# Performance work log

Hardware: AMD Instinct MI355X
Metric: run time of the kernel (lower is better)

## Reference

```python
import jax, jax.numpy as jnp
import numpy as np

B, N, M = 2, 4096, 1024
QD, CD, H, DH = 512, 768, 8, 64
SCALE = DH ** -0.5


def setup_inputs() -> dict:
    key = jax.random.key(0)
    ks = jax.random.split(key, 8)
    return {
        "x": jax.random.normal(ks[0], (B, N, QD), jnp.float32),
        "context": jax.random.normal(ks[1], (B, M, CD), jnp.float32),
        "adapt": jax.random.normal(ks[2], (B, N, H * DH), jnp.float32),
        "Wq": jax.random.normal(ks[3], (QD, H * DH), jnp.float32) * (QD ** -0.5),
        "Wk": jax.random.normal(ks[4], (CD, H * DH), jnp.float32) * (CD ** -0.5),
        "Wv": jax.random.normal(ks[5], (CD, H * DH), jnp.float32) * (CD ** -0.5),
        "Wo": jax.random.normal(ks[6], (H * DH, QD), jnp.float32) * ((H * DH) ** -0.5),
        "bo": jnp.zeros((QD,), jnp.float32),
    }


def _split_heads(t):
    # [b, n, h*d] -> [b, h, n, d]
    b, n, _ = t.shape
    return t.reshape(b, n, H, DH).transpose(0, 2, 1, 3)


def reference(x, context, adapt, Wq, Wk, Wv, Wo, bo):
    q = _split_heads(x @ Wq)          # [b,h,n,d]
    k = _split_heads(context @ Wk)    # [b,h,m,d]
    v = _split_heads(context @ Wv)    # [b,h,m,d]

    sim = jnp.einsum('bhid,bhjd->bhij', q, k) * SCALE  # [b,h,n,m]
    attn = jax.nn.softmax(sim, axis=-1)
    # NOTE: module averages raw logits (sim) over heads, not softmax probs
    attention_probs_avg = sim.mean(axis=1)             # [b,n,m]
    out = jnp.einsum('bhij,bhjd->bhid', attn, v)       # [b,h,n,d]

    # adapt-query pass reusing k, v
    qa = _split_heads(adapt)
    sim_a = jnp.einsum('bhid,bhjd->bhij', qa, k) * SCALE
    attn_a = jax.nn.softmax(sim_a, axis=-1)
    out = out + jnp.einsum('bhij,bhjd->bhid', attn_a, v)

    out = out.transpose(0, 2, 1, 3).reshape(B, N, H * DH)  # merge heads
    return (out @ Wo + bo, attention_probs_avg)
```

## Files before the change

### kernel.cpp

```cpp
#include <hip/hip_runtime.h>

typedef __attribute__((ext_vector_type(8))) short bh8;
typedef __attribute__((ext_vector_type(4))) float f4;
typedef __attribute__((ext_vector_type(4))) unsigned short us4;
typedef __attribute__((ext_vector_type(4))) unsigned int u32x4;

__device__ __forceinline__ unsigned short rne_bf16(float x) {
  unsigned int u = __builtin_bit_cast(unsigned int, x);
  u += 0x7fffu + ((u >> 16) & 1u);
  return (unsigned short)(u >> 16);
}

__device__ __forceinline__ unsigned int cvt_pk_bf16(float lo, float hi) {
  unsigned int r;
  asm("v_cvt_pk_bf16_f32 %0, %1, %2" : "=v"(r) : "v"(lo), "v"(hi));
  return r;
}

__device__ __forceinline__ void gl_lds16(const void* g, void* l) {
  __builtin_amdgcn_global_load_lds(
      (const __attribute__((address_space(1))) void*)g,
      (__attribute__((address_space(3))) void*)l, 16, 0, 0);
}

__global__ __launch_bounds__(256) void prep_kernel(
    const float* __restrict__ x, unsigned short* __restrict__ xb,
    const float* __restrict__ context, unsigned short* __restrict__ cb,
    const float* __restrict__ Wq, const float* __restrict__ Wk,
    const float* __restrict__ Wv, const float* __restrict__ Wo,
    unsigned short* __restrict__ WqT, unsigned short* __restrict__ WkvT,
    unsigned short* __restrict__ WoT) {
  const int bid = blockIdx.x, tid = threadIdx.x;
  if (bid < 1024) {
    const int n40 = (8192 * 512) / 4, n41 = (2048 * 768) / 4;
    const int total = n40 + n41, stride = 1024 * 256;
    for (int i = bid * 256 + tid; i < total; i += stride) {
      const float* in = (i < n40) ? x : context;
      unsigned short* out = (i < n40) ? xb : cb;
      const int j = (i < n40) ? i : (i - n40);
      f4 v = *(const f4*)(in + (long)j * 4);
      us4 o;
#pragma unroll
      for (int e = 0; e < 4; ++e) o[e] = rne_bf16(v[e]);
      *(us4*)(out + (long)j * 4) = o;
    }
    return;
  }
  int u = bid - 1024;
  const float* in;
  unsigned short* out;
  int K;
  if (u < 256)       { in = Wq; out = WqT;               K = 512; }
  else if (u < 640)  { u -= 256; in = Wk; out = WkvT;    K = 768; }
  else if (u < 1024) { u -= 640; in = Wv; out = WkvT + 512L * 768; K = 768; }
  else               { u -= 1024; in = Wo; out = WoT;    K = 512; }
  const int N = 512;
  const int n0 = (u & 15) * 32, k0 = (u >> 4) * 32;
  __shared__ float t[32][33];
  const int tx = tid & 31, ty = tid >> 5;
#pragma unroll
  for (int r = 0; r < 32; r += 8)
    t[ty + r][tx] = in[(long)(k0 + ty + r) * N + n0 + tx];
  __syncthreads();
#pragma unroll
  for (int r = 0; r < 32; r += 8)
    out[(long)(n0 + ty + r) * K + k0 + tx] = rne_bf16(t[tx][ty + r]);
}

template <int MODE>
__device__ __forceinline__ void gemm_body(
    const unsigned short* __restrict__ A, const unsigned short* __restrict__ Bt,
    void* __restrict__ Cv, int K, int lda, int ldb, int ldc,
    long astr, long bstr, long cstr, float scale, const float* __restrict__ bias,
    int bx, int by, int bz) {
  __shared__ unsigned short As[2][16 * 512];
  __shared__ unsigned short Bs[2][16 * 512];
  const int tid = threadIdx.x, w = tid >> 6, l = tid & 63;
  const int c = l & 15, g = l >> 4;
  const int m0 = by * 128, n0 = bx * 128;
  const unsigned short* Ab = A + (long)bz * astr;
  const unsigned short* Bb = Bt + (long)bz * bstr;

  auto stage = [&](int buf, int kt) {
#pragma unroll
    for (int s = 0; s < 4; ++s) {
      const int idx = w * 4 + s;
      const int row = ((idx >> 1) & 7) * 16 + c;
      const int col = kt * 64 + (idx & 1) * 32 + g * 8;
      gl_lds16(Ab + (long)(m0 + row) * lda + col, (char*)&As[buf][0] + idx * 1024);
      gl_lds16(Bb + (long)(n0 + row) * ldb + col, (char*)&Bs[buf][0] + idx * 1024);
    }
  };

  f4 acc[4][4];
#pragma unroll
  for (int i = 0; i < 4; ++i)
#pragma unroll
    for (int j = 0; j < 4; ++j) acc[i][j] = (f4){0.f, 0.f, 0.f, 0.f};

  const int nkt = K >> 6;
  stage(0, 0);
  asm volatile("s_waitcnt vmcnt(0)" ::: "memory");
  __syncthreads();

  for (int kt = 0; kt < nkt; ++kt) {
    const int cur = kt & 1;
    if (kt + 1 < nkt) stage(cur ^ 1, kt + 1);
#pragma unroll
    for (int kk = 0; kk < 2; ++kk) {
      bh8 af[4], bfr[4];
#pragma unroll
      for (int i = 0; i < 4; ++i) {
        af[i] = *(const bh8*)((const char*)&As[cur][0] + (((w >> 1) * 8 + i * 2 + kk) * 1024) + l * 16);
        bfr[i] = *(const bh8*)((const char*)&Bs[cur][0] + (((w & 1) * 8 + i * 2 + kk) * 1024) + l * 16);
      }
#pragma unroll
      for (int i = 0; i < 4; ++i)
#pragma unroll
        for (int j = 0; j < 4; ++j)
          acc[i][j] = __builtin_amdgcn_mfma_f32_16x16x32_bf16(af[i], bfr[j], acc[i][j], 0, 0, 0);
    }
    if (kt + 1 < nkt) {
      asm volatile("s_waitcnt vmcnt(0)" ::: "memory");
      __syncthreads();
    }
  }

  const int rbase = m0 + (w >> 1) * 64, cbase = n0 + (w & 1) * 64;
#pragma unroll
  for (int i = 0; i < 4; ++i)
#pragma unroll
    for (int j = 0; j < 4; ++j)
#pragma unroll
      for (int r = 0; r < 4; ++r) {
        const long row = rbase + i * 16 + g * 4 + r;
        const long col = cbase + j * 16 + c;
        const float v = acc[i][j][r];
        if (MODE == 0) {
          ((unsigned short*)Cv + (long)bz * cstr)[row * ldc + col] = rne_bf16(v * scale);
        } else if (MODE == 1) {
          ((float*)Cv + (long)bz * cstr)[row * ldc + col] = v * scale;
        } else {
          ((float*)Cv)[row * ldc + col] = v + bias[col];
        }
      }
}

__global__ __launch_bounds__(256, 2) void gemm_qkv(
    const unsigned short* __restrict__ xb, const unsigned short* __restrict__ WqT,
    unsigned short* __restrict__ Qb,
    const unsigned short* __restrict__ cb, const unsigned short* __restrict__ WkvT,
    unsigned short* __restrict__ KVb, float cexp) {
  const int bid = blockIdx.x;
  const unsigned short *A, *Bt;
  unsigned short* C;
  int K, ldb_, ldc_, bx, by;
  float sc;
  if (bid < 256) {
    A = xb; Bt = WqT; C = Qb; K = 512; ldb_ = 512; ldc_ = 512;
    bx = bid & 3; by = bid >> 2; sc = cexp;
  } else {
    const int u = bid - 256;
    A = cb; Bt = WkvT; C = KVb; K = 768; ldb_ = 768; ldc_ = 1024;
    bx = u & 7; by = u >> 3; sc = 1.f;
  }
  gemm_body<0>(A, Bt, C, K, K, ldb_, ldc_, 0, 0, 0, sc, nullptr, bx, by, 0);
}

__global__ __launch_bounds__(256, 2) void probs_vt(
    const unsigned short* __restrict__ Qb, const unsigned short* __restrict__ KVb,
    float* __restrict__ out1, unsigned short* __restrict__ VTb, float avg_scale) {
  const int bid = blockIdx.x;
  if (bid >= 512) {
    const int u = bid - 512;
    const int j0 = (u & 63) * 32, d0 = (u >> 6) * 32;
    __shared__ unsigned short t[32][34];
    const int tx = threadIdx.x & 31, ty = threadIdx.x >> 5;
#pragma unroll
    for (int r = 0; r < 32; r += 8)
      t[ty + r][tx] = KVb[(long)(j0 + ty + r) * 1024 + 512 + d0 + tx];
    __syncthreads();
#pragma unroll
    for (int r = 0; r < 32; r += 8)
      VTb[(long)(d0 + ty + r) * 2048 + j0 + tx] = t[tx][ty + r];
    return;
  }
  gemm_body<1>(Qb, KVb, out1, 512, 512, 1024, 1024,
               4096L * 512, 1024L * 1024, 4096L * 1024, avg_scale, nullptr,
               bid & 7, (bid >> 3) & 31, bid >> 8);
}

__global__ __launch_bounds__(256, 2) void gemm_out(
    const unsigned short* __restrict__ Ob, const unsigned short* __restrict__ WoT,
    float* __restrict__ out0, const float* __restrict__ bias) {
  gemm_body<2>(Ob, WoT, out0, 512, 512, 512, 512, 0, 0, 0, 1.f, bias,
               blockIdx.x, blockIdx.y, 0);
}

__global__ __launch_bounds__(256, 4) void attn_kernel(
    const unsigned short* __restrict__ Qb, const float* __restrict__ adapt,
    const unsigned short* __restrict__ KV, const unsigned short* __restrict__ VT,
    unsigned short* __restrict__ Ob) {
  __shared__ unsigned short Ks[2][8 * 512];
  __shared__ unsigned short Vs[2][8 * 512];
  const int qt = blockIdx.y, h = blockIdx.x, b = blockIdx.z;
  const int tid = threadIdx.x, w = tid >> 6, l = tid & 63;
  const int c = l & 15, g = l >> 4;
  const float CEXP = 0.18033688011112042f;

  const unsigned short* Kg = KV + ((long)b * 1024) * 1024 + h * 64;
  const unsigned short* Vg = VT + (long)h * 64 * 2048 + b * 1024;

  auto stage = [&](int buf, int jt0) {
#pragma unroll
    for (int s = 0; s < 2; ++s) {
      const int idx = w * 2 + s;
      const int row = (idx >> 1) * 16 + c;
      const int col = (idx & 1) * 32 + g * 8;
      gl_lds16(Kg + ((long)jt0 * 64 + row) * 1024 + col, (char*)&Ks[buf][0] + idx * 1024);
      gl_lds16(Vg + (long)row * 2048 + jt0 * 64 + col, (char*)&Vs[buf][0] + idx * 1024);
    }
  };

  stage(0, 0);

  const long qrow = (long)b * 4096 + qt * 64 + w * 16 + c;
  bh8 qf[2][2];
#pragma unroll
  for (int kk = 0; kk < 2; ++kk) {
    const int col = h * 64 + kk * 32 + g * 8;
    qf[0][kk] = *(const bh8*)(Qb + qrow * 512 + col);
    const float* ap = adapt + qrow * 512 + col;
    f4 x0 = *(const f4*)ap, x1 = *(const f4*)(ap + 4);
    bh8 t;
#pragma unroll
    for (int e = 0; e < 4; ++e) {
      t[e] = (short)rne_bf16(x0[e] * CEXP);
      t[e + 4] = (short)rne_bf16(x1[e] * CEXP);
    }
    qf[1][kk] = t;
  }

  f4 psum[2];
  f4 accv[2][4];
#pragma unroll
  for (int qs = 0; qs < 2; ++qs) {
    psum[qs] = (f4){0.f, 0.f, 0.f, 0.f};
#pragma unroll
    for (int dt = 0; dt < 4; ++dt) accv[qs][dt] = (f4){0.f, 0.f, 0.f, 0.f};
  }

  asm volatile("s_waitcnt vmcnt(0)" ::: "memory");
  __syncthreads();

  auto make_pf = [&](const f4& s2k, const f4& s2k1) -> bh8 {
    unsigned int p0 = cvt_pk_bf16(s2k[0], s2k[1]);
    unsigned int p1 = cvt_pk_bf16(s2k[2], s2k[3]);
    unsigned int q0 = cvt_pk_bf16(s2k1[0], s2k1[1]);
    unsigned int q1 = cvt_pk_bf16(s2k1[2], s2k1[3]);
    asm("v_permlane32_swap_b32 %0, %1" : "+v"(p0), "+v"(q0));
    asm("v_permlane16_swap_b32 %0, %1" : "+v"(p0), "+v"(q0));
    asm("v_permlane32_swap_b32 %0, %1" : "+v"(p1), "+v"(q1));
    asm("v_permlane16_swap_b32 %0, %1" : "+v"(p1), "+v"(q1));
    u32x4 u = {p0, p1, q0, q1};
    return __builtin_bit_cast(bh8, u);
  };

  for (int jt0 = 0; jt0 < 16; ++jt0) {
    const int cur = jt0 & 1;
    if (jt0 < 15) stage(cur ^ 1, jt0 + 1);

    f4 s0[4], s1[4];
    __builtin_amdgcn_s_setprio(1);
#pragma unroll
    for (int jt = 0; jt < 4; ++jt) {
      bh8 k0 = *(const bh8*)((const char*)&Ks[cur][0] + (jt * 2 + 0) * 1024 + l * 16);
      bh8 k1 = *(const bh8*)((const char*)&Ks[cur][0] + (jt * 2 + 1) * 1024 + l * 16);
      s0[jt] = (f4){0.f, 0.f, 0.f, 0.f};
      s0[jt] = __builtin_amdgcn_mfma_f32_16x16x32_bf16(k0, qf[0][0], s0[jt], 0, 0, 0);
      s0[jt] = __builtin_amdgcn_mfma_f32_16x16x32_bf16(k1, qf[0][1], s0[jt], 0, 0, 0);
      s1[jt] = (f4){0.f, 0.f, 0.f, 0.f};
      s1[jt] = __builtin_amdgcn_mfma_f32_16x16x32_bf16(k0, qf[1][0], s1[jt], 0, 0, 0);
      s1[jt] = __builtin_amdgcn_mfma_f32_16x16x32_bf16(k1, qf[1][1], s1[jt], 0, 0, 0);
    }
    __builtin_amdgcn_s_setprio(0);

#pragma unroll
    for (int jt = 0; jt < 4; ++jt)
#pragma unroll
      for (int r = 0; r < 4; ++r) {
        s0[jt][r] = __builtin_amdgcn_exp2f(s0[jt][r]);
        s1[jt][r] = __builtin_amdgcn_exp2f(s1[jt][r]);
      }
#pragma unroll
    for (int jt = 0; jt < 4; ++jt) { psum[0] += s0[jt]; psum[1] += s1[jt]; }

    bh8 pf0[2], pf1[2];
#pragma unroll
    for (int kk = 0; kk < 2; ++kk) {
      pf0[kk] = make_pf(s0[2 * kk], s0[2 * kk + 1]);
      pf1[kk] = make_pf(s1[2 * kk], s1[2 * kk + 1]);
    }

    __builtin_amdgcn_s_setprio(1);
#pragma unroll
    for (int dt = 0; dt < 4; ++dt) {
      bh8 v0 = *(const bh8*)((const char*)&Vs[cur][0] + (dt * 2 + 0) * 1024 + l * 16);
      bh8 v1 = *(const bh8*)((const char*)&Vs[cur][0] + (dt * 2 + 1) * 1024 + l * 16);
      accv[0][dt] = __builtin_amdgcn_mfma_f32_16x16x32_bf16(v0, pf0[0], accv[0][dt], 0, 0, 0);
      accv[0][dt] = __builtin_amdgcn_mfma_f32_16x16x32_bf16(v1, pf0[1], accv[0][dt], 0, 0, 0);
      accv[1][dt] = __builtin_amdgcn_mfma_f32_16x16x32_bf16(v0, pf1[0], accv[1][dt], 0, 0, 0);
      accv[1][dt] = __builtin_amdgcn_mfma_f32_16x16x32_bf16(v1, pf1[1], accv[1][dt], 0, 0, 0);
    }
    __builtin_amdgcn_s_setprio(0);

    if (jt0 < 15) {
      asm volatile("s_waitcnt vmcnt(0)" ::: "memory");
      __syncthreads();
    }
  }

  float l0 = (psum[0][0] + psum[0][1]) + (psum[0][2] + psum[0][3]);
  l0 += __shfl_xor(l0, 16); l0 += __shfl_xor(l0, 32);
  float l1 = (psum[1][0] + psum[1][1]) + (psum[1][2] + psum[1][3]);
  l1 += __shfl_xor(l1, 16); l1 += __shfl_xor(l1, 32);
  const float i0 = 1.0f / l0, i1 = 1.0f / l1;
  const long orow = (long)b * 4096 + qt * 64 + w * 16 + c;
#pragma unroll
  for (int dt = 0; dt < 4; ++dt) {
    float v0 = accv[0][dt][0] * i0 + accv[1][dt][0] * i1;
    float v1 = accv[0][dt][1] * i0 + accv[1][dt][1] * i1;
    float v2 = accv[0][dt][2] * i0 + accv[1][dt][2] * i1;
    float v3 = accv[0][dt][3] * i0 + accv[1][dt][3] * i1;
    uint2 o;
    o.x = cvt_pk_bf16(v0, v1);
    o.y = cvt_pk_bf16(v2, v3);
    *(uint2*)(Ob + orow * 512 + h * 64 + dt * 16 + g * 4) = o;
  }
}

extern "C" void kernel_launch(void* const* d_in, const int* in_sizes, int n_in,
                              void* d_out, int out_size, void* d_ws, size_t ws_size,
                              hipStream_t stream) {
  (void)in_sizes; (void)n_in; (void)out_size; (void)ws_size;
  const float* x       = (const float*)d_in[0];
  const float* context = (const float*)d_in[1];
  const float* adapt   = (const float*)d_in[2];
  const float* Wq      = (const float*)d_in[3];
  const float* Wk      = (const float*)d_in[4];
  const float* Wv      = (const float*)d_in[5];
  const float* Wo      = (const float*)d_in[6];
  const float* bo      = (const float*)d_in[7];
  float* out0 = (float*)d_out;
  float* out1 = out0 + (long)2 * 4096 * 512;

  const float CEXP = 0.18033688011112042f;
  const float AVG_SCALE = 0.015625f / CEXP;

  char* wp = (char*)d_ws;
  auto take = [&](long elems) { unsigned short* p = (unsigned short*)wp; wp += elems * 2; return p; };
  unsigned short* xb   = take(8192L * 512);
  unsigned short* cb   = take(2048L * 768);
  unsigned short* WqT  = take(512L * 512);
  unsigned short* WkvT = take(1024L * 768);
  unsigned short* WoT  = take(512L * 512);
  unsigned short* Qb   = take(8192L * 512);
  unsigned short* KVb  = take(2048L * 1024);
  unsigned short* VTb  = take(512L * 2048);
  unsigned short* Ob   = take(8192L * 512);

  prep_kernel<<<2304, 256, 0, stream>>>(x, xb, context, cb, Wq, Wk, Wv, Wo, WqT, WkvT, WoT);
  gemm_qkv<<<384, 256, 0, stream>>>(xb, WqT, Qb, cb, WkvT, KVb, CEXP);
  probs_vt<<<1536, 256, 0, stream>>>(Qb, KVb, out1, VTb, AVG_SCALE);
  attn_kernel<<<dim3(8, 64, 2), 256, 0, stream>>>(Qb, adapt, KVb, VTb, Ob);
  gemm_out<<<dim3(4, 64), 256, 0, stream>>>(Ob, WoT, out0, bo);
}
```

Measured before the change: 122.0 us.

## Use 128x64 GEMM tiles for projections and compute softmax row sums via MFMA

Adds a smaller-tile GEMM body (128x64 per block) for the QKV and output projections, doubling the block count and raising launch-bound occupancy to 3 blocks per SM, so a small grid fills more CUs. In attention, the per-row softmax denominators are now accumulated with an MFMA against a ones vector instead of VALU adds plus cross-lane shuffles, and V fragments are loaded up front. This trades extra MFMA work and lower per-block reuse for less VALU work and better CU fill.

```diff
diff --git a/kernel.cpp b/kernel.cpp
--- a/kernel.cpp
+++ b/kernel.cpp
@@ -146,25 +146,100 @@
       }
 }
 
-__global__ __launch_bounds__(256, 2) void gemm_qkv(
+template <int MODE>
+__device__ __forceinline__ void gemm_body64(
+    const unsigned short* __restrict__ A, const unsigned short* __restrict__ Bt,
+    void* __restrict__ Cv, int K, int lda, int ldb, int ldc,
+    float scale, const float* __restrict__ bias, int bx, int by) {
+  __shared__ unsigned short As[2][16 * 512];
+  __shared__ unsigned short Bs[2][8 * 512];
+  const int tid = threadIdx.x, w = tid >> 6, l = tid & 63;
+  const int c = l & 15, g = l >> 4;
+  const int m0 = by * 128, n0 = bx * 64;
+  const int wr = w & 1, wc = w >> 1;
+
+  auto stage = [&](int buf, int kt) {
+#pragma unroll
+    for (int s = 0; s < 6; ++s) {
+      const int idx = w * 6 + s;
+      if (idx < 16) {
+        const int row = (idx >> 1) * 16 + c;
+        const int col = kt * 64 + (idx & 1) * 32 + g * 8;
+        gl_lds16(A + (long)(m0 + row) * lda + col, (char*)&As[buf][0] + idx * 1024);
+      } else {
+        const int ib = idx - 16;
+        const int row = (ib >> 1) * 16 + c;
+        const int col = kt * 64 + (ib & 1) * 32 + g * 8;
+        gl_lds16(Bt + (long)(n0 + row) * ldb + col, (char*)&Bs[buf][0] + ib * 1024);
+      }
+    }
+  };
+
+  f4 acc[4][2];
+#pragma unroll
+  for (int i = 0; i < 4; ++i)
+#pragma unroll
+    for (int j = 0; j < 2; ++j) acc[i][j] = (f4){0.f, 0.f, 0.f, 0.f};
+
+  const int nkt = K >> 6;
+  stage(0, 0);
+  asm volatile("s_waitcnt vmcnt(0)" ::: "memory");
+  __syncthreads();
+
+  for (int kt = 0; kt < nkt; ++kt) {
+    const int cur = kt & 1;
+    if (kt + 1 < nkt) stage(cur ^ 1, kt + 1);
+#pragma unroll
+    for (int kk = 0; kk < 2; ++kk) {
+      bh8 af[4], bfr[2];
+#pragma unroll
+      for (int i = 0; i < 4; ++i)
+        af[i] = *(const bh8*)((const char*)&As[cur][0] + (((wr * 4 + i) * 2 + kk) * 1024) + l * 16);
+#pragma unroll
+      for (int j = 0; j < 2; ++j)
+        bfr[j] = *(const bh8*)((const char*)&Bs[cur][0] + (((wc * 2 + j) * 2 + kk) * 1024) + l * 16);
+#pragma unroll
+      for (int i = 0; i < 4; ++i)
+#pragma unroll
+        for (int j = 0; j < 2; ++j)
+          acc[i][j] = __builtin_amdgcn_mfma_f32_16x16x32_bf16(af[i], bfr[j], acc[i][j], 0, 0, 0);
+    }
+    if (kt + 1 < nkt) {
+      asm volatile("s_waitcnt vmcnt(0)" ::: "memory");
+      __syncthreads();
+    }
+  }
+
+  const int rbase = m0 + wr * 64, cbase = n0 + wc * 32;
+#pragma unroll
+  for (int i = 0; i < 4; ++i)
+#pragma unroll
+    for (int j = 0; j < 2; ++j)
+#pragma unroll
+      for (int r = 0; r < 4; ++r) {
+        const long row = rbase + i * 16 + g * 4 + r;
+        const long col = cbase + j * 16 + c;
+        const float v = acc[i][j][r];
+        if (MODE == 0) {
+          ((unsigned short*)Cv)[row * ldc + col] = rne_bf16(v * scale);
+        } else if (MODE == 2) {
+          ((float*)Cv)[row * ldc + col] = v + bias[col];
+        }
+      }
+}
+
+__global__ __launch_bounds__(256, 3) void gemm_qkv(
     const unsigned short* __restrict__ xb, const unsigned short* __restrict__ WqT,
     unsigned short* __restrict__ Qb,
     const unsigned short* __restrict__ cb, const unsigned short* __restrict__ WkvT,
     unsigned short* __restrict__ KVb, float cexp) {
   const int bid = blockIdx.x;
-  const unsigned short *A, *Bt;
-  unsigned short* C;
-  int K, ldb_, ldc_, bx, by;
-  float sc;
-  if (bid < 256) {
-    A = xb; Bt = WqT; C = Qb; K = 512; ldb_ = 512; ldc_ = 512;
-    bx = bid & 3; by = bid >> 2; sc = cexp;
+  if (bid < 512) {
+    gemm_body64<0>(xb, WqT, Qb, 512, 512, 512, 512, cexp, nullptr, bid & 7, bid >> 3);
   } else {
-    const int u = bid - 256;
-    A = cb; Bt = WkvT; C = KVb; K = 768; ldb_ = 768; ldc_ = 1024;
-    bx = u & 7; by = u >> 3; sc = 1.f;
-  }
-  gemm_body<0>(A, Bt, C, K, K, ldb_, ldc_, 0, 0, 0, sc, nullptr, bx, by, 0);
+    const int u = bid - 512;
+    gemm_body64<0>(cb, WkvT, KVb, 768, 768, 768, 1024, 1.f, nullptr, u & 15, u >> 4);
+  }
 }
 
 __global__ __launch_bounds__(256, 2) void probs_vt(
@@ -190,11 +265,11 @@
                bid & 7, (bid >> 3) & 31, bid >> 8);
 }
 
-__global__ __launch_bounds__(256, 2) void gemm_out(
+__global__ __launch_bounds__(256, 3) void gemm_out(
     const unsigned short* __restrict__ Ob, const unsigned short* __restrict__ WoT,
     float* __restrict__ out0, const float* __restrict__ bias) {
-  gemm_body<2>(Ob, WoT, out0, 512, 512, 512, 512, 0, 0, 0, 1.f, bias,
-               blockIdx.x, blockIdx.y, 0);
+  const int bid = blockIdx.x;
+  gemm_body64<2>(Ob, WoT, out0, 512, 512, 512, 512, 1.f, bias, bid & 7, bid >> 3);
 }
 
 __global__ __launch_bounds__(256, 4) void attn_kernel(
@@ -241,11 +316,14 @@
     qf[1][kk] = t;
   }
 
-  f4 psum[2];
+  const u32x4 ones_u = {0x3F803F80u, 0x3F803F80u, 0x3F803F80u, 0x3F803F80u};
+  const bh8 ones = __builtin_bit_cast(bh8, ones_u);
+
+  f4 psacc[2];
   f4 accv[2][4];
 #pragma unroll
   for (int qs = 0; qs < 2; ++qs) {
-    psum[qs] = (f4){0.f, 0.f, 0.f, 0.f};
+    psacc[qs] = (f4){0.f, 0.f, 0.f, 0.f};
 #pragma unroll
     for (int dt = 0; dt < 4; ++dt) accv[qs][dt] = (f4){0.f, 0.f, 0.f, 0.f};
   }
@@ -292,8 +370,6 @@
         s0[jt][r] = __builtin_amdgcn_exp2f(s0[jt][r]);
         s1[jt][r] = __builtin_amdgcn_exp2f(s1[jt][r]);
       }
-#pragma unroll
-    for (int jt = 0; jt < 4; ++jt) { psum[0] += s0[jt]; psum[1] += s1[jt]; }
 
     bh8 pf0[2], pf1[2];
 #pragma unroll
@@ -302,15 +378,25 @@
       pf1[kk] = make_pf(s1[2 * kk], s1[2 * kk + 1]);
     }
 
+    bh8 vf[4][2];
+#pragma unroll
+    for (int dt = 0; dt < 4; ++dt)
+#pragma unroll
+      for (int kk = 0; kk < 2; ++kk)
+        vf[dt][kk] = *(const bh8*)((const char*)&Vs[cur][0] + (dt * 2 + kk) * 1024 + l * 16);
+
+    psacc[0] = __builtin_amdgcn_mfma_f32_16x16x32_bf16(ones, pf0[0], psacc[0], 0, 0, 0);
+    psacc[0] = __builtin_amdgcn_mfma_f32_16x16x32_bf16(ones, pf0[1], psacc[0], 0, 0, 0);
+    psacc[1] = __builtin_amdgcn_mfma_f32_16x16x32_bf16(ones, pf1[0], psacc[1], 0, 0, 0);
+    psacc[1] = __builtin_amdgcn_mfma_f32_16x16x32_bf16(ones, pf1[1], psacc[1], 0, 0, 0);
+
     __builtin_amdgcn_s_setprio(1);
 #pragma unroll
     for (int dt = 0; dt < 4; ++dt) {
-      bh8 v0 = *(const bh8*)((const char*)&Vs[cur][0] + (dt * 2 + 0) * 1024 + l * 16);
-      bh8 v1 = *(const bh8*)((const char*)&Vs[cur][0] + (dt * 2 + 1) * 1024 + l * 16);
-      accv[0][dt] = __builtin_amdgcn_mfma_f32_16x16x32_bf16(v0, pf0[0], accv[0][dt], 0, 0, 0);
-      accv[0][dt] = __builtin_amdgcn_mfma_f32_16x16x32_bf16(v1, pf0[1], accv[0][dt], 0, 0, 0);
-      accv[1][dt] = __builtin_amdgcn_mfma_f32_16x16x32_bf16(v0, pf1[0], accv[1][dt], 0, 0, 0);
-      accv[1][dt] = __builtin_amdgcn_mfma_f32_16x16x32_bf16(v1, pf1[1], accv[1][dt], 0, 0, 0);
+      accv[0][dt] = __builtin_amdgcn_mfma_f32_16x16x32_bf16(vf[dt][0], pf0[0], accv[0][dt], 0, 0, 0);
+      accv[0][dt] = __builtin_amdgcn_mfma_f32_16x16x32_bf16(vf[dt][1], pf0[1], accv[0][dt], 0, 0, 0);
+      accv[1][dt] = __builtin_amdgcn_mfma_f32_16x16x32_bf16(vf[dt][0], pf1[0], accv[1][dt], 0, 0, 0);
+      accv[1][dt] = __builtin_amdgcn_mfma_f32_16x16x32_bf16(vf[dt][1], pf1[1], accv[1][dt], 0, 0, 0);
     }
     __builtin_amdgcn_s_setprio(0);
 
@@ -320,11 +406,7 @@
     }
   }
 
-  float l0 = (psum[0][0] + psum[0][1]) + (psum[0][2] + psum[0][3]);
-  l0 += __shfl_xor(l0, 16); l0 += __shfl_xor(l0, 32);
-  float l1 = (psum[1][0] + psum[1][1]) + (psum[1][2] + psum[1][3]);
-  l1 += __shfl_xor(l1, 16); l1 += __shfl_xor(l1, 32);
-  const float i0 = 1.0f / l0, i1 = 1.0f / l1;
+  const float i0 = 1.0f / psacc[0][0], i1 = 1.0f / psacc[1][0];
   const long orow = (long)b * 4096 + qt * 64 + w * 16 + c;
 #pragma unroll
   for (int dt = 0; dt < 4; ++dt) {
@@ -370,8 +452,8 @@
   unsigned short* Ob   = take(8192L * 512);
 
   prep_kernel<<<2304, 256, 0, stream>>>(x, xb, context, cb, Wq, Wk, Wv, Wo, WqT, WkvT, WoT);
-  gemm_qkv<<<384, 256, 0, stream>>>(xb, WqT, Qb, cb, WkvT, KVb, CEXP);
+  gemm_qkv<<<768, 256, 0, stream>>>(xb, WqT, Qb, cb, WkvT, KVb, CEXP);
   probs_vt<<<1536, 256, 0, stream>>>(Qb, KVb, out1, VTb, AVG_SCALE);
   attn_kernel<<<dim3(8, 64, 2), 256, 0, stream>>>(Qb, adapt, KVb, VTb, Ob);
-  gemm_out<<<dim3(4, 64), 256, 0, stream>>>(Ob, WoT, out0, bo);
-}
+  gemm_out<<<512, 256, 0, stream>>>(Ob, WoT, out0, bo);
+}
```

Result: faster. 118.7 us (-2.7%).
